# Performance work log

Measured on AMD Instinct MI355X. Metric: run time of the kernel, lower is better.

Reference implementation:

```python
import jax, jax.numpy as jnp
import numpy as np

# ---- static anchor construction (mirrors build_anchors + valid_index in __init__) ----
F_W, F_H, F_S = 50, 37, 16
SCALES = (8.0, 16.0, 24.0)
RATIOS = (0.5, 1.0, 2.0)
K1 = 400            # rp() top-k proposals fed to NMS
NMS_THRESH = 0.6
BN_EPS = 1e-5

def _build_anchors():
    anchors = []
    for y in range(F_H):
        for x in range(F_W):
            cx = x * F_S + F_S / 2.0
            cy = y * F_S + F_S / 2.0
            for r in RATIOS:           # 3 ratios x 3 scales = 9 anchors/cell (18 = 9*2 cls ch)
                for s in SCALES:
                    h = F_S * s * np.sqrt(r)
                    w = F_S * s / np.sqrt(r)
                    anchors.append([cx - w / 2, cy - h / 2, cx + w / 2, cy + h / 2])
    return np.asarray(anchors, dtype=np.float32)

_ANCH = _build_anchors()
_VALID = np.where((_ANCH[:, 0] >= 0) & (_ANCH[:, 1] >= 0) &
                  (_ANCH[:, 2] < F_W * F_S) & (_ANCH[:, 3] < F_H * F_S))[0]
VALID_ANCHOR = jnp.asarray(_ANCH[_VALID])   # [V, 4]
VALID_INDEX = jnp.asarray(_VALID)            # [V]


def _conv(x, w, b, pad):
    y = jax.lax.conv_general_dilated(x, w, (1, 1), [(pad, pad), (pad, pad)],
                                     dimension_numbers=('NCHW', 'OIHW', 'NCHW'))
    return y + b[None, :, None, None]


def _nms_keep(boxes, scores, thresh):
    """Greedy NMS over K1 boxes; returns bool keep mask aligned to input order."""
    n = boxes.shape[0]
    order = jnp.argsort(-scores)
    b = boxes[order]
    x1, y1, x2, y2 = b[:, 0], b[:, 1], b[:, 2], b[:, 3]
    area = (x2 - x1 + 1.0) * (y2 - y1 + 1.0)
    iw = jnp.clip(jnp.minimum(x2[:, None], x2[None, :]) - jnp.maximum(x1[:, None], x1[None, :]) + 1.0, 0.0)
    ih = jnp.clip(jnp.minimum(y2[:, None], y2[None, :]) - jnp.maximum(y1[:, None], y1[None, :]) + 1.0, 0.0)
    inter = iw * ih
    iou = inter / (area[:, None] + area[None, :] - inter)
    idx = jnp.arange(n)

    def body(i, supp):
        alive = ~supp[i]
        new = alive & (iou[i] > thresh) & (idx > i)
        return supp | new

    supp = jax.lax.fori_loop(0, n, body, jnp.zeros(n, dtype=bool))
    return jnp.zeros(n, dtype=bool).at[order].set(~supp)


def _rp_single(off_i, cls_i):
    """rp(): softmax fg score -> top-k1 -> box decode -> NMS keep mask."""
    off_v = off_i[VALID_INDEX]                       # [V, 4]
    cls_v = cls_i[VALID_INDEX]                       # [V, 2]
    score = jax.nn.softmax(cls_v, axis=1)[:, 1]
    top_s, top_idx = jax.lax.top_k(score, K1)
    a = VALID_ANCHOR[top_idx]
    t = off_v[top_idx]
    xa = (a[:, 0] + a[:, 2]) / 2
    ya = (a[:, 1] + a[:, 3]) / 2
    wa = a[:, 2] - a[:, 0] + 1.0
    ha = a[:, 3] - a[:, 1] + 1.0
    x = t[:, 0] * wa + xa
    y = t[:, 1] * ha + ya
    w = wa * jnp.exp(t[:, 2])
    h = ha * jnp.exp(t[:, 3])
    boxes = jnp.stack([x - w / 2, y - h / 2, x + w / 2, y + h / 2], axis=1)  # [K1, 4]
    keep = _nms_keep(jnp.trunc(boxes), top_s, NMS_THRESH)  # original casts to int before NMS
    return boxes, keep


def setup_inputs() -> dict:
    key = jax.random.key(0)
    ks = jax.random.split(key, 8)
    B = 8
    return {
        'feature': jax.random.normal(ks[0], (B, 512, F_H, F_W), jnp.float32),
        'md_w': jax.random.normal(ks[1], (512, 512, 3, 3), jnp.float32) * 0.02,
        'md_b': jax.random.normal(ks[2], (512,), jnp.float32) * 0.01,
        'bn_gamma': jnp.ones((512,), jnp.float32),
        'bn_beta': jnp.zeros((512,), jnp.float32),
        'cls_w': jax.random.normal(ks[3], (18, 512, 1, 1), jnp.float32) * 0.02,
        'cls_b': jax.random.normal(ks[4], (18,), jnp.float32) * 0.01,
        'off_w': jax.random.normal(ks[5], (36, 512, 1, 1), jnp.float32) * 0.02,
        'off_b': jax.random.normal(ks[6], (36,), jnp.float32) * 0.01,
    }


def reference(feature, md_w, md_b, bn_gamma, bn_beta, cls_w, cls_b, off_w, off_b):
    B = feature.shape[0]
    # more_deep: Conv3x3 -> BatchNorm (training-mode batch stats) -> ReLU
    out = _conv(feature, md_w, md_b, pad=1)
    mean = out.mean(axis=(0, 2, 3), keepdims=True)
    var = out.var(axis=(0, 2, 3), keepdims=True)
    out = bn_gamma[None, :, None, None] * (out - mean) * jax.lax.rsqrt(var + BN_EPS) + bn_beta[None, :, None, None]
    out = jax.nn.relu(out)
    # 1x1 heads, then permute(0,2,3,1).reshape as in predict()
    cls = _conv(out, cls_w, cls_b, pad=0)   # [B,18,H,W]
    off = _conv(out, off_w, off_b, pad=0)   # [B,36,H,W]
    cls_pred = cls.transpose(0, 2, 3, 1).reshape(B, -1, 2)   # [B, H*W*9, 2]
    offset_pred = off.transpose(0, 2, 3, 1).reshape(B, -1, 4)  # [B, H*W*9, 4]
    boxes, keep = jax.vmap(_rp_single)(offset_pred, cls_pred)  # [B,K1,4], [B,K1] bool
    return offset_pred, cls_pred, boxes, keep
```

## Files before the change

### kernel.cpp

```cpp
#include <hip/hip_runtime.h>
#include <cstdint>

#define BHW_ 14800
#define CHW_ 947200
#define A_   16650
#define OCLS 532800
#define OBOX 799200
#define OKEEP 812000
#define NSTEP 144

typedef unsigned int u32;
typedef unsigned long long u64;
typedef _Float16 f16x8 __attribute__((ext_vector_type(8)));
typedef float f32x4 __attribute__((ext_vector_type(4)));

union U8 { f16x8 v; u32 u[4]; };
union H2U { _Float16 f; unsigned short u; };

__device__ __forceinline__ unsigned int fkey(float f){
  unsigned int u = __float_as_uint(f);
  return (u & 0x80000000u) ? ~u : (u | 0x80000000u);
}

__device__ __forceinline__ void anchor_corners(int x, int y, int kk,
                                               float& ax1, float& ay1, float& ax2, float& ay2){
  int si = kk % 3, ri = kk / 3;
  double rv = (ri==0) ? 0.5 : ((ri==1) ? 1.0 : 2.0);
  double sr = sqrt(rv);
  double fs = 128.0 * (double)(si+1);
  double h = fs * sr, w = fs / sr;
  double cx = (double)(x*16 + 8), cy = (double)(y*16 + 8);
  ax1 = (float)(cx - w*0.5); ay1 = (float)(cy - h*0.5);
  ax2 = (float)(cx + w*0.5); ay2 = (float)(cy + h*0.5);
}

__global__ __launch_bounds__(256) void k_prep(const float* __restrict__ feat, const float* __restrict__ mdw,
                                              const float* __restrict__ cw, const float* __restrict__ cb,
                                              const float* __restrict__ ow, const float* __restrict__ ob,
                                              u32* __restrict__ Fp, _Float16* __restrict__ WfA,
                                              float* __restrict__ hwp, float* __restrict__ hb){
  int bid = blockIdx.x;
  if (bid < 8112){
    int q = bid*256 + threadIdx.x;
    int p4 = (q % 507)*4;
    int bc = q / 507;
    u32 outw[4];
    #pragma unroll
    for (int e = 0; e < 4; ++e){
      int padpos = p4 + e;
      int yp = padpos/52, xp = padpos - yp*52;
      float v = 0.f;
      int y = yp - 1, x = xp - 1;
      if ((unsigned)y < 37u && (unsigned)x < 50u) v = feat[(size_t)bc*1850 + y*50 + x];
      _Float16 h = (_Float16)v;
      _Float16 l = (_Float16)(v - (float)h);
      H2U hu, lu; hu.f = h; lu.f = l;
      outw[e] = ((u32)lu.u << 16) | (u32)hu.u;
    }
    *(uint4*)&Fp[(size_t)bc*2028 + p4] = *(uint4*)outw;
  } else if (bid < 9264){
    int u = (bid - 8112)*256 + threadIdx.x;
    int khw = u % 9;
    int v = u / 9;
    int o7  = v & 127;
    int l4g = (v >> 7) & 3;
    int ot  = (v >> 9) & 3;
    int cc  = v >> 11;
    int o = ot*128 + o7;
    int s = cc*9 + khw;
    f16x8 hi, lo;
    #pragma unroll
    for (int j = 0; j < 8; ++j){
      float val = mdw[(size_t)(o*512 + cc*32 + l4g*8 + j)*9 + khw];
      _Float16 h = (_Float16)val;
      hi[j] = h; lo[j] = (_Float16)(val - (float)h);
    }
    size_t base = ((size_t)(s*4 + ot)*1024 + (size_t)(l4g*2)*128 + o7)*8;
    *(f16x8*)&WfA[base] = hi;
    *(f16x8*)&WfA[base + 1024] = lo;
  } else {
    int t = (bid - 9264)*256 + threadIdx.x;
    if (t < 64) hb[t] = (t < 18) ? cb[t] : (t < 54 ? ob[t-18] : 0.f);
    int r = t & 63, ci = t >> 6;
    hwp[t] = (r < 18) ? cw[r*512 + ci] : (r < 54 ? ow[(r-18)*512 + ci] : 0.f);
  }
}

__global__ __launch_bounds__(512, 2) void k_conv3_mfma(const u32* __restrict__ Fp,
                                                       const _Float16* __restrict__ WfA,
                                                       const float* __restrict__ mdb,
                                                       float* __restrict__ out0){
  __shared__ _Float16 Abuf[2][8192];
  __shared__ _Float16 Bbuf[2][8192];
  const int tid = threadIdx.x;
  int flat = blockIdx.x;
  int xcd = flat & 7, sub = flat >> 3;
  int swz = xcd * 58 + sub;
  int otile = swz / 116;
  int ntile = swz - otile*116;

  const int bpos = tid & 127, kg8 = tid >> 7;
  int n = ntile*128 + bpos; if (n >= BHW_) n = BHW_ - 1;
  int nb = n/1850; int rem = n - nb*1850; int ny = rem/50; int nx = rem - ny*50;
  const u32* bbase = Fp + (size_t)(nb*512 + kg8*8)*2028 + (ny+1)*52 + (nx+1);

  u32 R[8];
  auto loadB = [&](int s){
    int cc = s/9, khw = s - cc*9;
    int dy = khw/3 - 1, dx = khw - (khw/3)*3 - 1;
    const u32* src = bbase + (size_t)cc*32*2028 + dy*52 + dx;
    #pragma unroll
    for (int i = 0; i < 8; ++i) R[i] = src[(size_t)i*2028];
  };
  auto writeB = [&](int cur){
    U8 hi, lo;
    #pragma unroll
    for (int p = 0; p < 4; ++p){
      u32 P0 = R[2*p], P1 = R[2*p+1];
      hi.u[p] = (P1 << 16) | (P0 & 0xFFFFu);
      lo.u[p] = (P0 >> 16) | (P1 & 0xFFFF0000u);
    }
    *(f16x8*)&Bbuf[cur][(size_t)((kg8*2 + 0)*128 + bpos)*8] = hi.v;
    *(f16x8*)&Bbuf[cur][(size_t)((kg8*2 + 1)*128 + bpos)*8] = lo.v;
  };
  auto stageA = [&](int s, int cur){
    const _Float16* g = WfA + ((size_t)(s*4 + otile)*1024 + tid)*8;
    _Float16* l = &Abuf[cur][(size_t)tid*8];
    __builtin_amdgcn_global_load_lds((const __attribute__((address_space(1))) void*)g,
                                     (__attribute__((address_space(3))) void*)l, 16, 0, 0);
    __builtin_amdgcn_global_load_lds((const __attribute__((address_space(1))) void*)(g + 4096),
                                     (__attribute__((address_space(3))) void*)(l + 4096), 16, 0, 0);
  };

  const int w = tid >> 6, lane = tid & 63;
  const int wm = w >> 2, wn = w & 3;
  const int l15 = lane & 15, l4 = lane >> 4;

  f32x4 acc[4][2] = {};

  auto compute = [&](int cur){
    f16x8 ah[4], al[4], bh[2], bl[2];
    #pragma unroll
    for (int mf = 0; mf < 4; ++mf){
      int m = wm*64 + mf*16 + l15;
      ah[mf] = *(const f16x8*)&Abuf[cur][(size_t)((l4*2 + 0)*128 + m)*8];
      al[mf] = *(const f16x8*)&Abuf[cur][(size_t)((l4*2 + 1)*128 + m)*8];
    }
    #pragma unroll
    for (int nf = 0; nf < 2; ++nf){
      int nn = wn*32 + nf*16 + l15;
      bh[nf] = *(const f16x8*)&Bbuf[cur][(size_t)((l4*2 + 0)*128 + nn)*8];
      bl[nf] = *(const f16x8*)&Bbuf[cur][(size_t)((l4*2 + 1)*128 + nn)*8];
    }
    #pragma unroll
    for (int mf = 0; mf < 4; ++mf)
      #pragma unroll
      for (int nf = 0; nf < 2; ++nf){
        acc[mf][nf] = __builtin_amdgcn_mfma_f32_16x16x32_f16(ah[mf], bh[nf], acc[mf][nf], 0,0,0);
        acc[mf][nf] = __builtin_amdgcn_mfma_f32_16x16x32_f16(ah[mf], bl[nf], acc[mf][nf], 0,0,0);
        acc[mf][nf] = __builtin_amdgcn_mfma_f32_16x16x32_f16(al[mf], bh[nf], acc[mf][nf], 0,0,0);
      }
  };

  loadB(0);
  stageA(0, 0);
  writeB(0);
  __syncthreads();

  int cur = 0;
  for (int s = 0; s < NSTEP; ++s){
    if (s + 1 < NSTEP){
      loadB(s+1);
      stageA(s+1, cur^1);
      __builtin_amdgcn_sched_barrier(0);
    }
    compute(cur);
    if (s + 1 < NSTEP) writeB(cur^1);
    __syncthreads();
    cur ^= 1;
  }

  #pragma unroll
  for (int nf = 0; nf < 2; ++nf){
    int ng = ntile*128 + wn*32 + nf*16 + l15;
    if (ng >= BHW_) continue;
    int b2 = ng/1850; int rem2 = ng - b2*1850;
    #pragma unroll
    for (int mf = 0; mf < 4; ++mf){
      int o0 = otile*128 + wm*64 + mf*16 + l4*4;
      #pragma unroll
      for (int r = 0; r < 4; ++r){
        out0[(size_t)b2*CHW_ + (size_t)(o0 + r)*1850 + rem2] = acc[mf][nf][r] + mdb[o0 + r];
      }
    }
  }
}

__global__ __launch_bounds__(256) void k_bnstats(const float* __restrict__ out0,
                                                 float* __restrict__ bnm, float* __restrict__ bnr){
  __shared__ double s1[256], s2[256];
  int c = blockIdx.x, tid = threadIdx.x;
  double a = 0.0, b = 0.0;
  for (int i = tid; i < BHW_; i += 256){
    int bb = i / 1850; int r = i - bb*1850;
    float v = out0[(size_t)bb*CHW_ + (size_t)c*1850 + r];
    a += (double)v; b += (double)v*(double)v;
  }
  s1[tid] = a; s2[tid] = b; __syncthreads();
  for (int off = 128; off; off >>= 1){
    if (tid < off){ s1[tid] += s1[tid+off]; s2[tid] += s2[tid+off]; }
    __syncthreads();
  }
  if (tid == 0){
    double m = s1[0] / 14800.0;
    double var = s2[0] / 14800.0 - m*m;
    bnm[c] = (float)m;
    bnr[c] = 1.0f / sqrtf((float)var + 1e-5f);
  }
}

__global__ __launch_bounds__(256) void k_heads(const float* __restrict__ out0, const float* __restrict__ hwp,
                                               const float* __restrict__ hb, const float* __restrict__ bnm,
                                               const float* __restrict__ bnr, const float* __restrict__ gamma,
                                               const float* __restrict__ beta, float* __restrict__ dout,
                                               u64* __restrict__ keys){
#pragma clang fp contract(off)
  __shared__ float As[16][64];
  __shared__ float Bs[16][64];
  __shared__ int sb[64], sy[64], sx[64];
  int tid = threadIdx.x; int ntile = blockIdx.x;
  if (tid < 64){
    int n = ntile*64 + tid;
    if (n < BHW_){ int b = n/1850; int r = n - b*1850; int y = r/50; sb[tid]=b; sy[tid]=y; sx[tid]=r - y*50; }
    else { sb[tid] = -1; sy[tid] = 0; sx[tid] = 0; }
  }
  __syncthreads();
  float acc[4][4] = {};
  const int tx = tid & 15, ty = tid >> 4;
  const int lci = tid >> 4, lo4 = (tid & 15) * 4;
  for (int ct = 0; ct < 32; ++ct){
    int cib = ct*16;
    float4 av = *(const float4*)(hwp + (cib + lci)*64 + lo4);
    float4 bv; float* bp = (float*)&bv;
    int cig = cib + lci;
    float gm = gamma[cig], mm = bnm[cig], rr = bnr[cig], bt = beta[cig];
    #pragma unroll
    for (int j = 0; j < 4; ++j){
      int nn = lo4 + j; int b = sb[nn];
      float v = 0.f;
      if (b >= 0){
        float x = out0[(size_t)b*CHW_ + (size_t)cig*1850 + sy[nn]*50 + sx[nn]];
        float y = gm * (x - mm);
        y = y * rr;
        y = y + bt;
        v = fmaxf(y, 0.f);
      }
      bp[j] = v;
    }
    __syncthreads();
    *(float4*)&As[lci][lo4] = av;
    *(float4*)&Bs[lci][lo4] = bv;
    __syncthreads();
    #pragma unroll
    for (int k = 0; k < 16; ++k){
      float4 a4 = *(const float4*)&As[k][ty*4];
      float4 b4 = *(const float4*)&Bs[k][tx*4];
      const float* ap = (const float*)&a4; const float* bq = (const float*)&b4;
      #pragma unroll
      for (int i = 0; i < 4; ++i)
        #pragma unroll
        for (int j = 0; j < 4; ++j)
          acc[i][j] = fmaf(ap[i], bq[j], acc[i][j]);
    }
  }
  #pragma unroll
  for (int i = 0; i < 4; ++i){
    int r = ty*4 + i;
    if (r >= 54) continue;
    float bias = hb[r];
    #pragma unroll
    for (int j = 0; j < 4; ++j){
      int nl = tx*4 + j;
      int b = sb[nl];
      if (b < 0) continue;
      int pos = sy[nl]*50 + sx[nl];
      float v = acc[i][j] + bias;
      if (r < 18){
        int kk = r >> 1, cc = r & 1;
        dout[OCLS + ((size_t)b*A_ + pos*9 + kk)*2 + cc] = v;
      } else {
        int r2 = r - 18, kk = r2 >> 2, cc = r2 & 3;
        dout[((size_t)b*A_ + pos*9 + kk)*4 + cc] = v;
      }
    }
  }
  if (ty < 5){
    #pragma unroll
    for (int i = 0; i < 4; i += 2){
      int r = ty*4 + i;
      if (r >= 18) continue;
      int kk = r >> 1;
      float b0 = hb[r], b1 = hb[r+1];
      #pragma unroll
      for (int j = 0; j < 4; ++j){
        int nl = tx*4 + j;
        int b = sb[nl];
        if (b < 0) continue;
        float c0 = acc[i][j] + b0;
        float c1 = acc[i+1][j] + b1;
        float d = c1 - c0;
        float ax1, ay1, ax2, ay2;
        anchor_corners(sx[nl], sy[nl], kk, ax1, ay1, ax2, ay2);
        bool valid = (ax1 >= 0.f) && (ay1 >= 0.f) && (ax2 < 800.f) && (ay2 < 592.f);
        unsigned a = (unsigned)(sy[nl]*50 + sx[nl])*9u + (unsigned)kk;
        u64 key = valid ? (((u64)fkey(d) << 32) | (u64)(~a)) : 0ull;
        keys[(size_t)b*A_ + a] = key;
      }
    }
  }
}

__global__ __launch_bounds__(1024) void k_post(const u64* __restrict__ keys,
                                               float* __restrict__ dout){
#pragma clang fp contract(off)
  __shared__ u32 hist[4096];
  __shared__ u32 sp[1024];
  __shared__ u64 selbuf[4096];
  __shared__ u64 stopk[400];
  __shared__ u32 adj32[6400];
  __shared__ float X1[400], Y1[400], X2[400], Y2[400], AR[400];
  __shared__ u32 ssup[13];
  __shared__ u32 s_t1, s_base1, s_t2, scnt;
  int b = blockIdx.x, tid = threadIdx.x;
  const u64* kb = keys + (size_t)b*A_;

  for (int i = tid; i < 4096; i += 1024) hist[i] = 0u;
  if (tid == 0) scnt = 0u;
  __syncthreads();
  for (int i = tid; i < A_; i += 1024){
    u64 k = kb[i];
    if (k) atomicAdd(&hist[(u32)(k >> 52)], 1u);
  }
  __syncthreads();
  {
    u32 p = hist[tid*4] + hist[tid*4+1] + hist[tid*4+2] + hist[tid*4+3];
    sp[tid] = p; __syncthreads();
    for (int off = 1; off < 1024; off <<= 1){
      u32 v = sp[tid] + ((tid + off < 1024) ? sp[tid + off] : 0u);
      __syncthreads(); sp[tid] = v; __syncthreads();
    }
    if (sp[tid] >= 400u && (tid == 1023 || sp[tid+1] < 400u)){
      u32 cum = (tid == 1023) ? 0u : sp[tid+1];
      for (int bb = tid*4 + 3; bb >= tid*4; --bb){
        cum += hist[bb];
        if (cum >= 400u){ s_t1 = (u32)bb; s_base1 = cum - hist[bb]; break; }
      }
    }
  }
  __syncthreads();
  const u32 t1 = s_t1;
  const u32 need2 = 400u - s_base1;

  __syncthreads();
  for (int i = tid; i < 4096; i += 1024) hist[i] = 0u;
  __syncthreads();
  for (int i = tid; i < A_; i += 1024){
    u64 k = kb[i];
    if (k && (u32)(k >> 52) == t1) atomicAdd(&hist[(u32)(k >> 40) & 0xFFFu], 1u);
  }
  __syncthreads();
  {
    u32 p = hist[tid*4] + hist[tid*4+1] + hist[tid*4+2] + hist[tid*4+3];
    sp[tid] = p; __syncthreads();
    for (int off = 1; off < 1024; off <<= 1){
      u32 v = sp[tid] + ((tid + off < 1024) ? sp[tid + off] : 0u);
      __syncthreads(); sp[tid] = v; __syncthreads();
    }
    if (sp[tid] >= need2 && (tid == 1023 || sp[tid+1] < need2)){
      u32 cum = (tid == 1023) ? 0u : sp[tid+1];
      for (int bb = tid*4 + 3; bb >= tid*4; --bb){
        cum += hist[bb];
        if (cum >= need2){ s_t2 = (u32)bb; break; }
      }
    }
  }
  __syncthreads();
  const u32 t2 = s_t2;

  for (int i = tid; i < A_; i += 1024){
    u64 k = kb[i];
    if (!k) continue;
    u32 top = (u32)(k >> 52);
    bool sel = (top > t1) || (top == t1 && ((u32)(k >> 40) & 0xFFFu) >= t2);
    if (sel){
      u32 pidx = atomicAdd(&scnt, 1u);
      if (pidx < 4096u) selbuf[pidx] = k;
    }
  }
  __syncthreads();
  int C = min((int)scnt, 4096);

  for (int i = tid; i < C; i += 1024){
    u64 my = selbuf[i];
    int c = 0;
    for (int j = 0; j < C; ++j) c += (selbuf[j] > my) ? 1 : 0;
    if (c < 400) stopk[c] = my;
  }
  __syncthreads();

  for (int i = tid; i < 6400; i += 1024) adj32[i] = 0u;
  if (tid < 400){
    u64 key = stopk[tid];
    unsigned a = ~(unsigned)(key & 0xFFFFFFFFull);
    int pos = a/9; int kk = a - pos*9;
    int y = pos/50; int x = pos - y*50;
    float ax1, ay1, ax2, ay2;
    anchor_corners(x, y, kk, ax1, ay1, ax2, ay2);
    float xa = (ax1 + ax2) * 0.5f;
    float ya = (ay1 + ay2) * 0.5f;
    float wa = ax2 - ax1 + 1.0f;
    float ha = ay2 - ay1 + 1.0f;
    const float* t = dout + ((size_t)b*A_ + a)*4;
    float t0 = t[0], t1f = t[1], t2f = t[2], t3 = t[3];
    float xc = t0 * wa + xa;
    float yc = t1f * ha + ya;
    float bw = wa * expf(t2f);
    float bh = ha * expf(t3);
    float bx1 = xc - bw*0.5f, by1 = yc - bh*0.5f;
    float bx2 = xc + bw*0.5f, by2 = yc + bh*0.5f;
    float* bo = dout + OBOX + ((size_t)b*400 + tid)*4;
    bo[0] = bx1; bo[1] = by1; bo[2] = bx2; bo[3] = by2;
    float tx1 = truncf(bx1), ty1 = truncf(by1), tx2 = truncf(bx2), ty2 = truncf(by2);
    X1[tid] = tx1; Y1[tid] = ty1; X2[tid] = tx2; Y2[tid] = ty2;
    AR[tid] = (tx2 - tx1 + 1.0f) * (ty2 - ty1 + 1.0f);
  }
  __syncthreads();
  for (int q = tid; q < 160000; q += 1024){
    int i = q / 400, j = q - i*400;
    if (j > i){
      float iw = fminf(X2[i], X2[j]) - fmaxf(X1[i], X1[j]) + 1.0f; iw = fmaxf(iw, 0.f);
      float ih = fminf(Y2[i], Y2[j]) - fmaxf(Y1[i], Y1[j]) + 1.0f; ih = fmaxf(ih, 0.f);
      float inter = iw * ih;
      float iou = inter / ((AR[i] + AR[j]) - inter);
      if (iou > 0.6f) atomicOr(&adj32[i*16 + (j >> 5)], 1u << (j & 31));
    }
  }
  __syncthreads();
  if (tid < 64){
    u32 sup = 0;
    for (int i = 0; i < 399; ++i){
      u32 a = (tid < 13) ? adj32[i*16 + tid] : 0u;
      u32 so = __shfl(sup, i >> 5);
      if (!((so >> (i & 31)) & 1u)) sup |= a;
    }
    if (tid < 13) ssup[tid] = sup;
  }
  __syncthreads();
  if (tid < 400)
    dout[OKEEP + (size_t)b*400 + tid] = ((ssup[tid >> 5] >> (tid & 31)) & 1u) ? 0.f : 1.f;
}

extern "C" void kernel_launch(void* const* d_in, const int* in_sizes, int n_in,
                              void* d_out, int out_size, void* d_ws, size_t ws_size,
                              hipStream_t stream){
  const float* feat  = (const float*)d_in[0];
  const float* mdw   = (const float*)d_in[1];
  const float* mdb   = (const float*)d_in[2];
  const float* gamma = (const float*)d_in[3];
  const float* beta  = (const float*)d_in[4];
  const float* clsw  = (const float*)d_in[5];
  const float* clsb  = (const float*)d_in[6];
  const float* offw  = (const float*)d_in[7];
  const float* offb  = (const float*)d_in[8];
  float* dout = (float*)d_out;
  float* ws = (float*)d_ws;

  float* out0 = ws;
  _Float16* WfA = (_Float16*)(out0 + 7577600);
  u32* Fp = (u32*)(out0 + 7577600 + 2359296);
  float* hwp = (float*)(Fp + 8306688);
  float* hb  = hwp + 32768;
  float* bnm = hb + 64;
  float* bnr = bnm + 512;
  u64* keys = (u64*)(bnr + 512);

  k_prep<<<dim3(9392), 256, 0, stream>>>(feat, mdw, clsw, clsb, offw, offb, Fp, WfA, hwp, hb);
  k_conv3_mfma<<<dim3(464), 512, 0, stream>>>(Fp, WfA, mdb, out0);
  k_bnstats<<<dim3(512), 256, 0, stream>>>(out0, bnm, bnr);
  k_heads<<<dim3(232), 256, 0, stream>>>(out0, hwp, hb, bnm, bnr, gamma, beta, dout, keys);
  k_post<<<dim3(8), 1024, 0, stream>>>(keys, dout);
}
```

Before: 389.5 us.

## Fuse BatchNorm statistics into conv epilogue using fixed-point atomics

Removes the separate BN statistics kernel, which re-read the whole conv output. Per-channel sum and sum-of-squares are now accumulated in the conv epilogue: values are converted to fixed-point integers, reduced with wave shuffles and shared-memory atomics, then combined per block with global 64-bit atomics. The heads kernel derives mean and rstd from those sums in shared memory. This saves one launch and a full pass over the activations, but adds atomic traffic and a fixed-point precision and overflow risk.

Measured after the change: 382.0 us. Within noise of the previous version (-1.9%).

```diff
diff --git a/kernel.cpp b/kernel.cpp
--- a/kernel.cpp
+++ b/kernel.cpp
@@ -38,7 +38,8 @@
                                               const float* __restrict__ cw, const float* __restrict__ cb,
                                               const float* __restrict__ ow, const float* __restrict__ ob,
                                               u32* __restrict__ Fp, _Float16* __restrict__ WfA,
-                                              float* __restrict__ hwp, float* __restrict__ hb){
+                                              float* __restrict__ hwp, float* __restrict__ hb,
+                                              u64* __restrict__ Sg){
   int bid = blockIdx.x;
   if (bid < 8112){
     int q = bid*256 + threadIdx.x;
@@ -81,6 +82,7 @@
   } else {
     int t = (bid - 9264)*256 + threadIdx.x;
     if (t < 64) hb[t] = (t < 18) ? cb[t] : (t < 54 ? ob[t-18] : 0.f);
+    if (t < 1024) Sg[t] = 0ull;
     int r = t & 63, ci = t >> 6;
     hwp[t] = (r < 18) ? cw[r*512 + ci] : (r < 54 ? ow[(r-18)*512 + ci] : 0.f);
   }
@@ -89,10 +91,13 @@
 __global__ __launch_bounds__(512, 2) void k_conv3_mfma(const u32* __restrict__ Fp,
                                                        const _Float16* __restrict__ WfA,
                                                        const float* __restrict__ mdb,
-                                                       float* __restrict__ out0){
+                                                       float* __restrict__ out0,
+                                                       u64* __restrict__ Sg){
   __shared__ _Float16 Abuf[2][8192];
   __shared__ _Float16 Bbuf[2][8192];
+  __shared__ u64 Sred[256];
   const int tid = threadIdx.x;
+  if (tid < 256) Sred[tid] = 0ull;
   int flat = blockIdx.x;
   int xcd = flat & 7, sub = flat >> 3;
   int swz = xcd * 58 + sub;
@@ -194,41 +199,57 @@
       }
     }
   }
-}
-
-__global__ __launch_bounds__(256) void k_bnstats(const float* __restrict__ out0,
-                                                 float* __restrict__ bnm, float* __restrict__ bnr){
-  __shared__ double s1[256], s2[256];
-  int c = blockIdx.x, tid = threadIdx.x;
-  double a = 0.0, b = 0.0;
-  for (int i = tid; i < BHW_; i += 256){
-    int bb = i / 1850; int r = i - bb*1850;
-    float v = out0[(size_t)bb*CHW_ + (size_t)c*1850 + r];
-    a += (double)v; b += (double)v*(double)v;
-  }
-  s1[tid] = a; s2[tid] = b; __syncthreads();
-  for (int off = 128; off; off >>= 1){
-    if (tid < off){ s1[tid] += s1[tid+off]; s2[tid] += s2[tid+off]; }
-    __syncthreads();
-  }
-  if (tid == 0){
-    double m = s1[0] / 14800.0;
-    double var = s2[0] / 14800.0 - m*m;
-    bnm[c] = (float)m;
-    bnr[c] = 1.0f / sqrtf((float)var + 1e-5f);
-  }
+  #pragma unroll
+  for (int mf = 0; mf < 4; ++mf){
+    int o0 = otile*128 + wm*64 + mf*16 + l4*4;
+    #pragma unroll
+    for (int r = 0; r < 4; ++r){
+      float bias = mdb[o0 + r];
+      long long s = 0, s2 = 0;
+      #pragma unroll
+      for (int nf = 0; nf < 2; ++nf){
+        int ng = ntile*128 + wn*32 + nf*16 + l15;
+        if (ng < BHW_){
+          double v = (double)(acc[mf][nf][r] + bias);
+          s  += __double2ll_rn(v * 16777216.0);
+          s2 += __double2ll_rn(v * v * 1073741824.0);
+        }
+      }
+      #pragma unroll
+      for (int m2 = 1; m2 < 16; m2 <<= 1){
+        s  += __shfl_xor(s,  m2, 64);
+        s2 += __shfl_xor(s2, m2, 64);
+      }
+      if (l15 == 0){
+        int cloc = wm*64 + mf*16 + l4*4 + r;
+        atomicAdd(&Sred[cloc*2],   (u64)s);
+        atomicAdd(&Sred[cloc*2+1], (u64)s2);
+      }
+    }
+  }
+  __syncthreads();
+  if (tid < 256) atomicAdd(&Sg[otile*256 + tid], Sred[tid]);
 }
 
 __global__ __launch_bounds__(256) void k_heads(const float* __restrict__ out0, const float* __restrict__ hwp,
-                                               const float* __restrict__ hb, const float* __restrict__ bnm,
-                                               const float* __restrict__ bnr, const float* __restrict__ gamma,
+                                               const float* __restrict__ hb, const u64* __restrict__ Sg,
+                                               const float* __restrict__ gamma,
                                                const float* __restrict__ beta, float* __restrict__ dout,
                                                u64* __restrict__ keys){
 #pragma clang fp contract(off)
   __shared__ float As[16][64];
   __shared__ float Bs[16][64];
+  __shared__ float bnmL[512], bnrL[512];
   __shared__ int sb[64], sy[64], sx[64];
   int tid = threadIdx.x; int ntile = blockIdx.x;
+  for (int c = tid; c < 512; c += 256){
+    double s  = (double)(long long)Sg[c*2]   / 16777216.0;
+    double s2 = (double)(long long)Sg[c*2+1] / 1073741824.0;
+    double m = s / 14800.0;
+    double var = s2 / 14800.0 - m*m;
+    bnmL[c] = (float)m;
+    bnrL[c] = 1.0f / sqrtf((float)var + 1e-5f);
+  }
   if (tid < 64){
     int n = ntile*64 + tid;
     if (n < BHW_){ int b = n/1850; int r = n - b*1850; int y = r/50; sb[tid]=b; sy[tid]=y; sx[tid]=r - y*50; }
@@ -243,7 +264,7 @@
     float4 av = *(const float4*)(hwp + (cib + lci)*64 + lo4);
     float4 bv; float* bp = (float*)&bv;
     int cig = cib + lci;
-    float gm = gamma[cig], mm = bnm[cig], rr = bnr[cig], bt = beta[cig];
+    float gm = gamma[cig], mm = bnmL[cig], rr = bnrL[cig], bt = beta[cig];
     #pragma unroll
     for (int j = 0; j < 4; ++j){
       int nn = lo4 + j; int b = sb[nn];
@@ -480,13 +501,11 @@
   u32* Fp = (u32*)(out0 + 7577600 + 2359296);
   float* hwp = (float*)(Fp + 8306688);
   float* hb  = hwp + 32768;
-  float* bnm = hb + 64;
-  float* bnr = bnm + 512;
-  u64* keys = (u64*)(bnr + 512);
-
-  k_prep<<<dim3(9392), 256, 0, stream>>>(feat, mdw, clsw, clsb, offw, offb, Fp, WfA, hwp, hb);
-  k_conv3_mfma<<<dim3(464), 512, 0, stream>>>(Fp, WfA, mdb, out0);
-  k_bnstats<<<dim3(512), 256, 0, stream>>>(out0, bnm, bnr);
-  k_heads<<<dim3(232), 256, 0, stream>>>(out0, hwp, hb, bnm, bnr, gamma, beta, dout, keys);
+  u64* Sg = (u64*)(hb + 64);
+  u64* keys = Sg + 1024;
+
+  k_prep<<<dim3(9392), 256, 0, stream>>>(feat, mdw, clsw, clsb, offw, offb, Fp, WfA, hwp, hb, Sg);
+  k_conv3_mfma<<<dim3(464), 512, 0, stream>>>(Fp, WfA, mdb, out0, Sg);
+  k_heads<<<dim3(232), 256, 0, stream>>>(out0, hwp, hb, Sg, gamma, beta, dout, keys);
   k_post<<<dim3(8), 1024, 0, stream>>>(keys, dout);
 }
```
